# Kernel optimization log

Hardware: AMD Instinct MI355X
Metric: run time of the kernel (lower is better)

## Reference

```python
import jax, jax.numpy as jnp
import numpy as np

H = 64          # hidden_size
IN = 6          # input_size
PREDICT = 10    # predict_size


def _lstm_cell(x_t, h, c, Wih, Whh, bih, bhh):
    # PyTorch gate order: i, f, g, o ; gates = x W_ih^T + b_ih + h W_hh^T + b_hh
    g = x_t @ Wih.T + bih + h @ Whh.T + bhh            # [B, 4H]
    i, f, gg, o = jnp.split(g, 4, axis=-1)
    c_new = jax.nn.sigmoid(f) * c + jax.nn.sigmoid(i) * jnp.tanh(gg)
    h_new = jax.nn.sigmoid(o) * jnp.tanh(c_new)
    return h_new, c_new


def setup_inputs() -> dict:
    key = jax.random.key(0)
    ks = jax.random.split(key, 12)
    B, T = 4096, 1024
    s = 1.0 / np.sqrt(H)  # torch default uniform init bound
    u = lambda k, shape: jax.random.uniform(k, shape, jnp.float32, -s, s)
    return {
        "x": jax.random.normal(ks[0], (B, T, IN), jnp.float32),
        "W_ih0": u(ks[1], (4 * H, IN)),
        "W_hh0": u(ks[2], (4 * H, H)),
        "b_ih0": u(ks[3], (4 * H,)),
        "b_hh0": u(ks[4], (4 * H,)),
        "W_ih1": u(ks[5], (4 * H, H)),
        "W_hh1": u(ks[6], (4 * H, H)),
        "b_ih1": u(ks[7], (4 * H,)),
        "b_hh1": u(ks[8], (4 * H,)),
        "fc_w": u(ks[9], (IN, H)),
        "fc_b": u(ks[10], (IN,)),
    }


def reference(x, W_ih0, W_hh0, b_ih0, b_hh0, W_ih1, W_hh1, b_ih1, b_hh1, fc_w, fc_b):
    B = x.shape[0]
    zeros = jnp.zeros((B, H), x.dtype)
    init = (zeros, zeros, zeros, zeros)  # h0, c0, h1, c1

    def stacked_step(carry, x_t):
        h0, c0, h1, c1 = carry
        h0, c0 = _lstm_cell(x_t, h0, c0, W_ih0, W_hh0, b_ih0, b_hh0)
        h1, c1 = _lstm_cell(h0, h1, c1, W_ih1, W_hh1, b_ih1, b_hh1)
        return (h0, c0, h1, c1), None

    # Encoder: scan over time (batch_first -> transpose to [T, B, IN])
    carry, _ = jax.lax.scan(stacked_step, init, jnp.swapaxes(x, 0, 1))

    def dec_step(state, _):
        dec_in, c = state
        c, _ = stacked_step(c, dec_in)
        pred = c[0 + 2] @ fc_w.T + fc_b  # top-layer h -> [B, IN]
        return (pred, c), pred

    dec_in0 = x[:, -1, :]
    _, preds = jax.lax.scan(dec_step, (dec_in0, carry), None, length=PREDICT)
    return jnp.swapaxes(preds, 0, 1)  # [B, PREDICT, IN]
```

## Files before the change

kernel.cpp:

```cpp
#include <hip/hip_runtime.h>

#define T_SEQ   1024
#define INDIM   6
#define HDIM    64
#define NPRED   10
#define CHNK    128
#define S0      72
#define NROWS   16

typedef __bf16         bf16x8 __attribute__((ext_vector_type(8)));
typedef float          f32x4  __attribute__((ext_vector_type(4)));
typedef float          f32x2  __attribute__((ext_vector_type(2)));
typedef unsigned short us4    __attribute__((ext_vector_type(4)));

#define MFMA16(a, b, c) __builtin_amdgcn_mfma_f32_16x16x32_bf16((a), (b), (c), 0, 0, 0)

static __device__ __forceinline__ float bf2f(unsigned short b) {
  union { unsigned int u; float f; } v; v.u = ((unsigned int)b) << 16; return v.f;
}
static __device__ __forceinline__ unsigned short f2bf(float f) {
  union { __bf16 b; unsigned short u; } v; v.b = (__bf16)f; return v.u;
}

template <bool F32>
__global__ __launch_bounds__(512, 2)
void lstm2_pipe(const void* __restrict__ xv,
                const void* __restrict__ Wih0v,
                const void* __restrict__ Whh0v,
                const void* __restrict__ bih0v,
                const void* __restrict__ bhh0v,
                const void* __restrict__ Wih1v,
                const void* __restrict__ Whh1v,
                const void* __restrict__ bih1v,
                const void* __restrict__ bhh1v,
                const void* __restrict__ fcwv,
                const void* __restrict__ fcbv,
                void* __restrict__ outv)
{
  {
    const unsigned short* w0u = (const unsigned short*)Wih0v;
    int votes = 0;
#pragma unroll
    for (int i = 0; i < 16; ++i) {
      const unsigned e = (w0u[2 * i] >> 7) & 0xFF;
      votes += (e >= 0x80 || e <= 0x40) ? 1 : 0;
    }
    if ((votes >= 4) != F32) return;
  }

  __shared__ __align__(16) unsigned short A0[2][NROWS * S0];
  __shared__ __align__(16) unsigned short A1[2][NROWS * S0];
  __shared__ __align__(16) unsigned short XB2[NROWS * CHNK * 8];
  __shared__ __align__(16) unsigned short XD[NROWS * 8];
  __shared__ __align__(16) unsigned short ZPAD[8];
  __shared__ __align__(16) unsigned short FCW[INDIM * HDIM];
  __shared__ float FCB[INDIM];

  const int tid   = threadIdx.x;
  const int lane  = tid & 63;
  const int wave  = tid >> 6;
  const bool isA  = (wave < 4);
  const int  wv4  = wave & 3;
  const int  q    = lane >> 4;
  const int  n    = lane & 15;
  const int  u    = 16 * wv4 + n;
  const int rbase = blockIdx.x * NROWS;

  {
    unsigned short* p0 = &A0[0][0];
    unsigned short* p1 = &A1[0][0];
    for (int i = tid; i < 2 * NROWS * S0; i += 512) { p0[i] = 0; p1[i] = 0; }
    for (int i = tid; i < NROWS * 8; i += 512) XD[i] = 0;
    if (tid < 8) ZPAD[tid] = 0;
  }
  for (int i = tid; i < INDIM * HDIM; i += 512) {
    if constexpr (F32) FCW[i] = f2bf(((const float*)fcwv)[i]);
    else               FCW[i] = ((const unsigned short*)fcwv)[i];
  }
  if (tid < INDIM) {
    if constexpr (F32) FCB[tid] = ((const float*)fcbv)[tid];
    else               FCB[tid] = bf2f(((const unsigned short*)fcbv)[tid]);
  }

  auto ld1 = [&](const void* p, int i) -> float {
    if constexpr (F32) return ((const float*)p)[i];
    else               return bf2f(((const unsigned short*)p)[i]);
  };
  auto ld8 = [&](const void* W, int off) -> bf16x8 {
    union { unsigned short us[8]; bf16x8 v; } t;
    if constexpr (F32) {
      const float* p = (const float*)W + off;
#pragma unroll
      for (int j = 0; j < 8; ++j) t.us[j] = f2bf(p[j]);
    } else {
      t.v = *(const bf16x8*)((const unsigned short*)W + off);
    }
    return t.v;
  };

  auto load_chunk = [&](int t0c) {
    for (int c = tid; c < NROWS * CHNK; c += 512) {
      const int row = c >> 7;
      const int t   = c & (CHNK - 1);
      int4 o;
      if constexpr (F32) {
        const float* p = (const float*)xv + ((size_t)(rbase + row) * T_SEQ + (t0c + t)) * INDIM;
        const float2 v0 = *(const float2*)(p);
        const float2 v1 = *(const float2*)(p + 2);
        const float2 v2 = *(const float2*)(p + 4);
        union { unsigned short us[8]; int4 v; } tt;
        tt.us[0] = f2bf(v0.x); tt.us[1] = f2bf(v0.y);
        tt.us[2] = f2bf(v1.x); tt.us[3] = f2bf(v1.y);
        tt.us[4] = f2bf(v2.x); tt.us[5] = f2bf(v2.y);
        tt.us[6] = 0;          tt.us[7] = 0;
        o = tt.v;
      } else {
        const unsigned short* p = (const unsigned short*)xv
            + ((size_t)(rbase + row) * T_SEQ + (t0c + t)) * INDIM;
        o.x = *(const unsigned int*)(p);
        o.y = *(const unsigned int*)(p + 2);
        o.z = *(const unsigned int*)(p + 4);
        o.w = 0;
      }
      *(int4*)((char*)XB2 + (((size_t)row * CHNK) + (t ^ (row & 7))) * 16) = o;
    }
  };

  load_chunk(0);

  const int dxr = tid / INDIM;
  const int dxk = tid - dxr * INDIM;

  __syncthreads();

  const int aOff  = n * S0 + 8 * q;
  const int hOffW = n * S0 + 16 * wv4 + 4 * q;
  const int bOff  = 16 * wv4 + 4 * q;

  auto xsrc_at = [&](int tc) -> const char* {
    return (q == 0)
        ? ((const char*)XB2 + (((size_t)n * CHNK) + (tc ^ (n & 7))) * 16)
        : (const char*)ZPAD;
  };

  f32x2 cc2[2]; cc2[0] = (f32x2){0.f, 0.f}; cc2[1] = (f32x2){0.f, 0.f};

  auto ldbias = [&](const void* b1, const void* b2, int gt) -> f32x4 {
    f32x4 r;
#pragma unroll
    for (int j = 0; j < 4; ++j)
      r[j] = ld1(b1, 64 * gt + bOff + j) + ld1(b2, 64 * gt + bOff + j);
    return r;
  };

  const f32x2 C1   = {-1.442695040888963f, -1.442695040888963f};
  const f32x2 C2   = {-2.885390081777927f, -2.885390081777927f};
  const f32x2 onep = {1.0f, 1.0f};

  auto act4 = [&](const f32x4 gI, const f32x4 gF, const f32x4 gG, const f32x4 gO,
                  unsigned short* dst) {
    unsigned int w2[2];
#pragma unroll
    for (int p = 0; p < 2; ++p) {
      f32x2 vI, vF, vG, vO;
      vI.x = gI[2 * p]; vI.y = gI[2 * p + 1];
      vF.x = gF[2 * p]; vF.y = gF[2 * p + 1];
      vG.x = gG[2 * p]; vG.y = gG[2 * p + 1];
      vO.x = gO[2 * p]; vO.y = gO[2 * p + 1];
      const f32x2 aF = vF * C1;
      const f32x2 aI = vI * C1;
      const f32x2 aG = vG * C2;
      const f32x2 aO = vO * C1;
      f32x2 Ae, Be, Ge, Oe;
      Ae.x = __builtin_amdgcn_exp2f(aF.x); Ae.y = __builtin_amdgcn_exp2f(aF.y);
      Be.x = __builtin_amdgcn_exp2f(aI.x); Be.y = __builtin_amdgcn_exp2f(aI.y);
      Ge.x = __builtin_amdgcn_exp2f(aG.x); Ge.y = __builtin_amdgcn_exp2f(aG.y);
      Oe.x = __builtin_amdgcn_exp2f(aO.x); Oe.y = __builtin_amdgcn_exp2f(aO.y);
      const f32x2 M1 = (onep + Be) * (onep + Ge);
      const f32x2 t2 = onep + Ae;
      const f32x2 nm = cc2[p] * M1 + (onep - Ge) * t2;
      const f32x2 den = t2 * M1;
      f32x2 rd; rd.x = __builtin_amdgcn_rcpf(den.x); rd.y = __builtin_amdgcn_rcpf(den.y);
      const f32x2 cn = nm * rd;
      cc2[p] = cn;
      const f32x2 aE = cn * C2;
      f32x2 Ee; Ee.x = __builtin_amdgcn_exp2f(aE.x); Ee.y = __builtin_amdgcn_exp2f(aE.y);
      const f32x2 dh = (onep + Ee) * (onep + Oe);
      f32x2 rh; rh.x = __builtin_amdgcn_rcpf(dh.x); rh.y = __builtin_amdgcn_rcpf(dh.y);
      const f32x2 hv = (onep - Ee) * rh;
      w2[p] = (unsigned int)f2bf(hv.x) | ((unsigned int)f2bf(hv.y) << 16);
    }
    uint2 pk; pk.x = w2[0]; pk.y = w2[1];
    *(uint2*)(dst + hOffW) = pk;
  };

  unsigned short* H0 = &A0[0][0];
  unsigned short* H1 = &A1[1][0];

  if (isA) {
    bf16x8 WA[12]; f32x4 bvA[4];
#pragma unroll
    for (int gt = 0; gt < 4; ++gt) {
      const int col = 64 * gt + u;
      WA[gt * 3 + 0] = ld8(Whh0v, col * HDIM + 8 * q);
      WA[gt * 3 + 1] = ld8(Whh0v, col * HDIM + 32 + 8 * q);
      union { unsigned short us[8]; bf16x8 v; } t2;
#pragma unroll
      for (int j = 0; j < 8; ++j) t2.us[j] = 0;
      if (q == 0) {
#pragma unroll
        for (int j = 0; j < INDIM; ++j) t2.us[j] = f2bf(ld1(Wih0v, col * INDIM + j));
      }
      WA[gt * 3 + 2] = t2.v;
      bvA[gt] = ldbias(bih0v, bhh0v, gt);
    }

    int t0v = 0;
    for (int i = 0; i <= T_SEQ; ++i) {
      if (i > 0 && i < T_SEQ && (i & (CHNK - 1)) == 0) {
        load_chunk(i);
        __syncthreads();
        t0v = i;
      }
      const int cur = i & 1;
      if (i < T_SEQ) {
        const unsigned short* A0c = &A0[cur][0];
        unsigned short*       A0n = &A0[cur ^ 1][0];
        const bf16x8 f0 = *(const bf16x8*)(A0c + aOff);
        const bf16x8 f1 = *(const bf16x8*)(A0c + aOff + 32);
        const bf16x8 f2 = *(const bf16x8*)(xsrc_at(i - t0v));
        __builtin_amdgcn_s_setprio(1);
        f32x4 g0 = MFMA16(WA[0], f0, bvA[0]); g0 = MFMA16(WA[1],  f1, g0); g0 = MFMA16(WA[2],  f2, g0);
        f32x4 g1 = MFMA16(WA[3], f0, bvA[1]); g1 = MFMA16(WA[4],  f1, g1); g1 = MFMA16(WA[5],  f2, g1);
        f32x4 g2 = MFMA16(WA[6], f0, bvA[2]); g2 = MFMA16(WA[7],  f1, g2); g2 = MFMA16(WA[8],  f2, g2);
        f32x4 g3 = MFMA16(WA[9], f0, bvA[3]); g3 = MFMA16(WA[10], f1, g3); g3 = MFMA16(WA[11], f2, g3);
        __builtin_amdgcn_s_setprio(0);
        act4(g0, g1, g2, g3, A0n);
      }
      __syncthreads();
    }
    if (tid < 96)
      XD[dxr * 8 + dxk] = XB2[((size_t)dxr * CHNK + (127 ^ (dxr & 7))) * 8 + dxk];
    __syncthreads();
    for (int d = 0; d < NPRED; ++d) {
      const bf16x8 fa0 = *(const bf16x8*)(H0 + aOff);
      const bf16x8 fa1 = *(const bf16x8*)(H0 + aOff + 32);
      const bf16x8 fa2 = *(const bf16x8*)((q == 0) ? ((const char*)XD + n * 16)
                                                   : (const char*)ZPAD);
      __syncthreads();
      {
        f32x4 g0 = MFMA16(WA[0], fa0, bvA[0]); g0 = MFMA16(WA[1],  fa1, g0); g0 = MFMA16(WA[2],  fa2, g0);
        f32x4 g1 = MFMA16(WA[3], fa0, bvA[1]); g1 = MFMA16(WA[4],  fa1, g1); g1 = MFMA16(WA[5],  fa2, g1);
        f32x4 g2 = MFMA16(WA[6], fa0, bvA[2]); g2 = MFMA16(WA[7],  fa1, g2); g2 = MFMA16(WA[8],  fa2, g2);
        f32x4 g3 = MFMA16(WA[9], fa0, bvA[3]); g3 = MFMA16(WA[10], fa1, g3); g3 = MFMA16(WA[11], fa2, g3);
        act4(g0, g1, g2, g3, H0);
      }
      __syncthreads();
      __syncthreads();
      if (tid < 96) {
        const unsigned short* h1row = H1 + dxr * S0;
        const int4* hp = (const int4*)h1row;
        const int4* wp = (const int4*)(&FCW[dxk * HDIM]);
        float s = FCB[dxk];
#pragma unroll
        for (int i8 = 0; i8 < 8; ++i8) {
          const int4 hv = hp[i8];
          const int4 wv2 = wp[i8];
          const unsigned int hu[4] = {(unsigned)hv.x, (unsigned)hv.y, (unsigned)hv.z, (unsigned)hv.w};
          const unsigned int wu[4] = {(unsigned)wv2.x, (unsigned)wv2.y, (unsigned)wv2.z, (unsigned)wv2.w};
#pragma unroll
          for (int k2 = 0; k2 < 4; ++k2) {
            union { unsigned int uu; float ff; } hl, hh2, wl, wh;
            hl.uu = hu[k2] << 16; hh2.uu = hu[k2] & 0xFFFF0000u;
            wl.uu = wu[k2] << 16; wh.uu  = wu[k2] & 0xFFFF0000u;
            s += hl.ff * wl.ff + hh2.ff * wh.ff;
          }
        }
        const unsigned short pb = f2bf(s);
        const size_t idx = (size_t)(rbase + dxr) * (NPRED * INDIM) + (size_t)d * INDIM + dxk;
        if constexpr (F32) ((float*)outv)[idx] = s;
        else               ((unsigned short*)outv)[idx] = pb;
        XD[dxr * 8 + dxk] = pb;
      }
      __syncthreads();
    }
  } else {
    bf16x8 WB[16]; f32x4 bvB[4];
#pragma unroll
    for (int gt = 0; gt < 4; ++gt) {
      const int col = 64 * gt + u;
      WB[gt * 4 + 0] = ld8(Wih1v, col * HDIM + 8 * q);
      WB[gt * 4 + 1] = ld8(Wih1v, col * HDIM + 32 + 8 * q);
      WB[gt * 4 + 2] = ld8(Whh1v, col * HDIM + 8 * q);
      WB[gt * 4 + 3] = ld8(Whh1v, col * HDIM + 32 + 8 * q);
      bvB[gt] = ldbias(bih1v, bhh1v, gt);
    }

    for (int i = 0; i <= T_SEQ; ++i) {
      if (i > 0 && i < T_SEQ && (i & (CHNK - 1)) == 0) {
        load_chunk(i);
        __syncthreads();
      }
      const int cur = i & 1;
      if (i >= 1) {
        const unsigned short* A0c = &A0[cur][0];
        const unsigned short* A1c = &A1[cur][0];
        unsigned short*       A1n = &A1[cur ^ 1][0];
        const bf16x8 h0a = *(const bf16x8*)(A0c + aOff);
        const bf16x8 h0b = *(const bf16x8*)(A0c + aOff + 32);
        const bf16x8 r0  = *(const bf16x8*)(A1c + aOff);
        const bf16x8 r1  = *(const bf16x8*)(A1c + aOff + 32);
        __builtin_amdgcn_s_setprio(1);
        f32x4 g0 = MFMA16(WB[0],  h0a, bvB[0]); g0 = MFMA16(WB[1],  h0b, g0); g0 = MFMA16(WB[2],  r0, g0); g0 = MFMA16(WB[3],  r1, g0);
        f32x4 g1 = MFMA16(WB[4],  h0a, bvB[1]); g1 = MFMA16(WB[5],  h0b, g1); g1 = MFMA16(WB[6],  r0, g1); g1 = MFMA16(WB[7],  r1, g1);
        f32x4 g2 = MFMA16(WB[8],  h0a, bvB[2]); g2 = MFMA16(WB[9],  h0b, g2); g2 = MFMA16(WB[10], r0, g2); g2 = MFMA16(WB[11], r1, g2);
        f32x4 g3 = MFMA16(WB[12], h0a, bvB[3]); g3 = MFMA16(WB[13], h0b, g3); g3 = MFMA16(WB[14], r0, g3); g3 = MFMA16(WB[15], r1, g3);
        __builtin_amdgcn_s_setprio(0);
        act4(g0, g1, g2, g3, A1n);
      }
      __syncthreads();
    }
    __syncthreads();
    for (int d = 0; d < NPRED; ++d) {
      const bf16x8 fr0 = *(const bf16x8*)(H1 + aOff);
      const bf16x8 fr1 = *(const bf16x8*)(H1 + aOff + 32);
      __syncthreads();
      __syncthreads();
      {
        const bf16x8 h0a = *(const bf16x8*)(H0 + aOff);
        const bf16x8 h0b = *(const bf16x8*)(H0 + aOff + 32);
        f32x4 g0 = MFMA16(WB[0],  h0a, bvB[0]); g0 = MFMA16(WB[1],  h0b, g0); g0 = MFMA16(WB[2],  fr0, g0); g0 = MFMA16(WB[3],  fr1, g0);
        f32x4 g1 = MFMA16(WB[4],  h0a, bvB[1]); g1 = MFMA16(WB[5],  h0b, g1); g1 = MFMA16(WB[6],  fr0, g1); g1 = MFMA16(WB[7],  fr1, g1);
        f32x4 g2 = MFMA16(WB[8],  h0a, bvB[2]); g2 = MFMA16(WB[9],  h0b, g2); g2 = MFMA16(WB[10], fr0, g2); g2 = MFMA16(WB[11], fr1, g2);
        f32x4 g3 = MFMA16(WB[12], h0a, bvB[3]); g3 = MFMA16(WB[13], h0b, g3); g3 = MFMA16(WB[14], fr0, g3); g3 = MFMA16(WB[15], fr1, g3);
        act4(g0, g1, g2, g3, H1);
      }
      __syncthreads();
      __syncthreads();
    }
  }
}

extern "C" void kernel_launch(void* const* d_in, const int* in_sizes, int n_in,
                              void* d_out, int out_size, void* d_ws, size_t ws_size,
                              hipStream_t stream) {
  (void)in_sizes; (void)n_in; (void)d_ws; (void)ws_size; (void)out_size;
  const void* x    = d_in[0];
  const void* Wih0 = d_in[1];
  const void* Whh0 = d_in[2];
  const void* bih0 = d_in[3];
  const void* bhh0 = d_in[4];
  const void* Wih1 = d_in[5];
  const void* Whh1 = d_in[6];
  const void* bih1 = d_in[7];
  const void* bhh1 = d_in[8];
  const void* fcw  = d_in[9];
  const void* fcb  = d_in[10];
  lstm2_pipe<true><<<dim3(4096 / NROWS), dim3(512), 0, stream>>>(
      x, Wih0, Whh0, bih0, bhh0, Wih1, Whh1, bih1, bhh1, fcw, fcb, d_out);
  lstm2_pipe<false><<<dim3(4096 / NROWS), dim3(512), 0, stream>>>(
      x, Wih0, Whh0, bih0, bhh0, Wih1, Whh1, bih1, bhh1, fcw, fcb, d_out);
}
```

Before: 873.0 us.

## Collapse each LSTM layer into one wave with windowed ring-buffer synchronization

Each 16-row block now runs on two waves (128 threads) instead of eight. One wave computes all 256 gate columns of layer 0 and the other all columns of layer 1, with every weight fragment held in registers. Layer 0 writes its hidden states into a 16-deep shared ring, and the two layers meet at a block barrier only once per 8-step window, with layer 1 lagging one window behind. This removes the per-timestep __syncthreads that the eight-wave split needed. The cost is 4x more serial MFMA and activation work per wave, lower in-block parallelism, and heavier register pressure, with fewer threads available to hide latency.

```diff
diff --git a/kernel.cpp b/kernel.cpp
--- a/kernel.cpp
+++ b/kernel.cpp
@@ -4,16 +4,18 @@
 #define INDIM   6
 #define HDIM    64
 #define NPRED   10
-#define CHNK    128
+#define CHNK    64
 #define S0      72
 #define NROWS   16
+#define RD      16
+#define WIN     8
 
 typedef __bf16         bf16x8 __attribute__((ext_vector_type(8)));
 typedef float          f32x4  __attribute__((ext_vector_type(4)));
 typedef float          f32x2  __attribute__((ext_vector_type(2)));
-typedef unsigned short us4    __attribute__((ext_vector_type(4)));
 
 #define MFMA16(a, b, c) __builtin_amdgcn_mfma_f32_16x16x32_bf16((a), (b), (c), 0, 0, 0)
+#define MEMBAR() asm volatile("" ::: "memory")
 
 static __device__ __forceinline__ float bf2f(unsigned short b) {
   union { unsigned int u; float f; } v; v.u = ((unsigned int)b) << 16; return v.f;
@@ -23,7 +25,7 @@
 }
 
 template <bool F32>
-__global__ __launch_bounds__(512, 2)
+__global__ __launch_bounds__(128, 1)
 void lstm2_pipe(const void* __restrict__ xv,
                 const void* __restrict__ Wih0v,
                 const void* __restrict__ Whh0v,
@@ -48,9 +50,10 @@
     if ((votes >= 4) != F32) return;
   }
 
-  __shared__ __align__(16) unsigned short A0[2][NROWS * S0];
-  __shared__ __align__(16) unsigned short A1[2][NROWS * S0];
+  __shared__ __align__(16) unsigned short RING[RD * NROWS * S0];
+  __shared__ __align__(16) unsigned short H1B[2 * NROWS * S0];
   __shared__ __align__(16) unsigned short XB2[NROWS * CHNK * 8];
+  __shared__ __align__(16) float BIAS1[4 * HDIM];
   __shared__ __align__(16) unsigned short XD[NROWS * 8];
   __shared__ __align__(16) unsigned short ZPAD[8];
   __shared__ __align__(16) unsigned short FCW[INDIM * HDIM];
@@ -58,29 +61,10 @@
 
   const int tid   = threadIdx.x;
   const int lane  = tid & 63;
-  const int wave  = tid >> 6;
-  const bool isA  = (wave < 4);
-  const int  wv4  = wave & 3;
+  const bool isA  = (tid < 64);
   const int  q    = lane >> 4;
   const int  n    = lane & 15;
-  const int  u    = 16 * wv4 + n;
   const int rbase = blockIdx.x * NROWS;
-
-  {
-    unsigned short* p0 = &A0[0][0];
-    unsigned short* p1 = &A1[0][0];
-    for (int i = tid; i < 2 * NROWS * S0; i += 512) { p0[i] = 0; p1[i] = 0; }
-    for (int i = tid; i < NROWS * 8; i += 512) XD[i] = 0;
-    if (tid < 8) ZPAD[tid] = 0;
-  }
-  for (int i = tid; i < INDIM * HDIM; i += 512) {
-    if constexpr (F32) FCW[i] = f2bf(((const float*)fcwv)[i]);
-    else               FCW[i] = ((const unsigned short*)fcwv)[i];
-  }
-  if (tid < INDIM) {
-    if constexpr (F32) FCB[tid] = ((const float*)fcbv)[tid];
-    else               FCB[tid] = bf2f(((const unsigned short*)fcbv)[tid]);
-  }
 
   auto ld1 = [&](const void* p, int i) -> float {
     if constexpr (F32) return ((const float*)p)[i];
@@ -98,9 +82,69 @@
     return t.v;
   };
 
-  auto load_chunk = [&](int t0c) {
-    for (int c = tid; c < NROWS * CHNK; c += 512) {
-      const int row = c >> 7;
+  {
+    const int4 z = {0, 0, 0, 0};
+    for (int i = tid; i < (2 * NROWS * S0) / 8; i += 128) ((int4*)H1B)[i] = z;
+    if (tid < (NROWS * 8) / 8) ((int4*)XD)[tid] = z;
+    if (tid < 8) ZPAD[tid] = 0;
+  }
+  for (int i = tid; i < 4 * HDIM; i += 128) BIAS1[i] = ld1(bih1v, i) + ld1(bhh1v, i);
+  for (int i = tid; i < INDIM * HDIM; i += 128) {
+    if constexpr (F32) FCW[i] = f2bf(((const float*)fcwv)[i]);
+    else               FCW[i] = ((const unsigned short*)fcwv)[i];
+  }
+  if (tid < INDIM) {
+    if constexpr (F32) FCB[tid] = ((const float*)fcbv)[tid];
+    else               FCB[tid] = bf2f(((const unsigned short*)fcbv)[tid]);
+  }
+
+  const int aOff = n * S0 + 8 * q;
+  const int hW   = n * S0 + 4 * q;
+
+  const f32x2 C1   = {-1.442695040888963f, -1.442695040888963f};
+  const f32x2 C2   = {-2.885390081777927f, -2.885390081777927f};
+  const f32x2 onep = {1.0f, 1.0f};
+
+  auto act4 = [&](const f32x4 gI, const f32x4 gF, const f32x4 gG, const f32x4 gO,
+                  unsigned short* dst, f32x2* cc) {
+    unsigned int w2[2];
+#pragma unroll
+    for (int p = 0; p < 2; ++p) {
+      f32x2 vI, vF, vG, vO;
+      vI.x = gI[2 * p]; vI.y = gI[2 * p + 1];
+      vF.x = gF[2 * p]; vF.y = gF[2 * p + 1];
+      vG.x = gG[2 * p]; vG.y = gG[2 * p + 1];
+      vO.x = gO[2 * p]; vO.y = gO[2 * p + 1];
+      const f32x2 aF = vF * C1;
+      const f32x2 aI = vI * C1;
+      const f32x2 aG = vG * C2;
+      const f32x2 aO = vO * C1;
+      f32x2 Ae, Be, Ge, Oe;
+      Ae.x = __builtin_amdgcn_exp2f(aF.x); Ae.y = __builtin_amdgcn_exp2f(aF.y);
+      Be.x = __builtin_amdgcn_exp2f(aI.x); Be.y = __builtin_amdgcn_exp2f(aI.y);
+      Ge.x = __builtin_amdgcn_exp2f(aG.x); Ge.y = __builtin_amdgcn_exp2f(aG.y);
+      Oe.x = __builtin_amdgcn_exp2f(aO.x); Oe.y = __builtin_amdgcn_exp2f(aO.y);
+      const f32x2 M1 = (onep + Be) * (onep + Ge);
+      const f32x2 t2 = onep + Ae;
+      const f32x2 nm = cc[p] * M1 + (onep - Ge) * t2;
+      const f32x2 den = t2 * M1;
+      f32x2 rd; rd.x = __builtin_amdgcn_rcpf(den.x); rd.y = __builtin_amdgcn_rcpf(den.y);
+      const f32x2 cn = nm * rd;
+      cc[p] = cn;
+      const f32x2 aE = cn * C2;
+      f32x2 Ee; Ee.x = __builtin_amdgcn_exp2f(aE.x); Ee.y = __builtin_amdgcn_exp2f(aE.y);
+      const f32x2 dh = (onep + Ee) * (onep + Oe);
+      f32x2 rh; rh.x = __builtin_amdgcn_rcpf(dh.x); rh.y = __builtin_amdgcn_rcpf(dh.y);
+      const f32x2 hv = (onep - Ee) * rh;
+      w2[p] = (unsigned int)f2bf(hv.x) | ((unsigned int)f2bf(hv.y) << 16);
+    }
+    uint2 pk; pk.x = w2[0]; pk.y = w2[1];
+    *(uint2*)(dst + hW) = pk;
+  };
+
+  auto stage = [&](int t0c) {
+    for (int c = lane; c < NROWS * CHNK; c += 64) {
+      const int row = c >> 6;
       const int t   = c & (CHNK - 1);
       int4 o;
       if constexpr (F32) {
@@ -124,144 +168,183 @@
       }
       *(int4*)((char*)XB2 + (((size_t)row * CHNK) + (t ^ (row & 7))) * 16) = o;
     }
+    MEMBAR();
   };
 
-  load_chunk(0);
-
-  const int dxr = tid / INDIM;
-  const int dxk = tid - dxr * INDIM;
-
-  __syncthreads();
-
-  const int aOff  = n * S0 + 8 * q;
-  const int hOffW = n * S0 + 16 * wv4 + 4 * q;
-  const int bOff  = 16 * wv4 + 4 * q;
-
-  auto xsrc_at = [&](int tc) -> const char* {
-    return (q == 0)
-        ? ((const char*)XB2 + (((size_t)n * CHNK) + (tc ^ (n & 7))) * 16)
-        : (const char*)ZPAD;
-  };
-
-  f32x2 cc2[2]; cc2[0] = (f32x2){0.f, 0.f}; cc2[1] = (f32x2){0.f, 0.f};
-
-  auto ldbias = [&](const void* b1, const void* b2, int gt) -> f32x4 {
-    f32x4 r;
-#pragma unroll
-    for (int j = 0; j < 4; ++j)
-      r[j] = ld1(b1, 64 * gt + bOff + j) + ld1(b2, 64 * gt + bOff + j);
-    return r;
-  };
-
-  const f32x2 C1   = {-1.442695040888963f, -1.442695040888963f};
-  const f32x2 C2   = {-2.885390081777927f, -2.885390081777927f};
-  const f32x2 onep = {1.0f, 1.0f};
-
-  auto act4 = [&](const f32x4 gI, const f32x4 gF, const f32x4 gG, const f32x4 gO,
-                  unsigned short* dst) {
-    unsigned int w2[2];
-#pragma unroll
-    for (int p = 0; p < 2; ++p) {
-      f32x2 vI, vF, vG, vO;
-      vI.x = gI[2 * p]; vI.y = gI[2 * p + 1];
-      vF.x = gF[2 * p]; vF.y = gF[2 * p + 1];
-      vG.x = gG[2 * p]; vG.y = gG[2 * p + 1];
-      vO.x = gO[2 * p]; vO.y = gO[2 * p + 1];
-      const f32x2 aF = vF * C1;
-      const f32x2 aI = vI * C1;
-      const f32x2 aG = vG * C2;
-      const f32x2 aO = vO * C1;
-      f32x2 Ae, Be, Ge, Oe;
-      Ae.x = __builtin_amdgcn_exp2f(aF.x); Ae.y = __builtin_amdgcn_exp2f(aF.y);
-      Be.x = __builtin_amdgcn_exp2f(aI.x); Be.y = __builtin_amdgcn_exp2f(aI.y);
-      Ge.x = __builtin_amdgcn_exp2f(aG.x); Ge.y = __builtin_amdgcn_exp2f(aG.y);
-      Oe.x = __builtin_amdgcn_exp2f(aO.x); Oe.y = __builtin_amdgcn_exp2f(aO.y);
-      const f32x2 M1 = (onep + Be) * (onep + Ge);
-      const f32x2 t2 = onep + Ae;
-      const f32x2 nm = cc2[p] * M1 + (onep - Ge) * t2;
-      const f32x2 den = t2 * M1;
-      f32x2 rd; rd.x = __builtin_amdgcn_rcpf(den.x); rd.y = __builtin_amdgcn_rcpf(den.y);
-      const f32x2 cn = nm * rd;
-      cc2[p] = cn;
-      const f32x2 aE = cn * C2;
-      f32x2 Ee; Ee.x = __builtin_amdgcn_exp2f(aE.x); Ee.y = __builtin_amdgcn_exp2f(aE.y);
-      const f32x2 dh = (onep + Ee) * (onep + Oe);
-      f32x2 rh; rh.x = __builtin_amdgcn_rcpf(dh.x); rh.y = __builtin_amdgcn_rcpf(dh.y);
-      const f32x2 hv = (onep - Ee) * rh;
-      w2[p] = (unsigned int)f2bf(hv.x) | ((unsigned int)f2bf(hv.y) << 16);
-    }
-    uint2 pk; pk.x = w2[0]; pk.y = w2[1];
-    *(uint2*)(dst + hOffW) = pk;
-  };
-
-  unsigned short* H0 = &A0[0][0];
-  unsigned short* H1 = &A1[1][0];
-
   if (isA) {
-    bf16x8 WA[12]; f32x4 bvA[4];
-#pragma unroll
-    for (int gt = 0; gt < 4; ++gt) {
-      const int col = 64 * gt + u;
-      WA[gt * 3 + 0] = ld8(Whh0v, col * HDIM + 8 * q);
-      WA[gt * 3 + 1] = ld8(Whh0v, col * HDIM + 32 + 8 * q);
-      union { unsigned short us[8]; bf16x8 v; } t2;
-#pragma unroll
-      for (int j = 0; j < 8; ++j) t2.us[j] = 0;
-      if (q == 0) {
-#pragma unroll
-        for (int j = 0; j < INDIM; ++j) t2.us[j] = f2bf(ld1(Wih0v, col * INDIM + j));
-      }
-      WA[gt * 3 + 2] = t2.v;
-      bvA[gt] = ldbias(bih0v, bhh0v, gt);
-    }
-
-    int t0v = 0;
-    for (int i = 0; i <= T_SEQ; ++i) {
-      if (i > 0 && i < T_SEQ && (i & (CHNK - 1)) == 0) {
-        load_chunk(i);
-        __syncthreads();
-        t0v = i;
-      }
-      const int cur = i & 1;
-      if (i < T_SEQ) {
-        const unsigned short* A0c = &A0[cur][0];
-        unsigned short*       A0n = &A0[cur ^ 1][0];
-        const bf16x8 f0 = *(const bf16x8*)(A0c + aOff);
-        const bf16x8 f1 = *(const bf16x8*)(A0c + aOff + 32);
-        const bf16x8 f2 = *(const bf16x8*)(xsrc_at(i - t0v));
-        __builtin_amdgcn_s_setprio(1);
-        f32x4 g0 = MFMA16(WA[0], f0, bvA[0]); g0 = MFMA16(WA[1],  f1, g0); g0 = MFMA16(WA[2],  f2, g0);
-        f32x4 g1 = MFMA16(WA[3], f0, bvA[1]); g1 = MFMA16(WA[4],  f1, g1); g1 = MFMA16(WA[5],  f2, g1);
-        f32x4 g2 = MFMA16(WA[6], f0, bvA[2]); g2 = MFMA16(WA[7],  f1, g2); g2 = MFMA16(WA[8],  f2, g2);
-        f32x4 g3 = MFMA16(WA[9], f0, bvA[3]); g3 = MFMA16(WA[10], f1, g3); g3 = MFMA16(WA[11], f2, g3);
-        __builtin_amdgcn_s_setprio(0);
-        act4(g0, g1, g2, g3, A0n);
-      }
-      __syncthreads();
-    }
-    if (tid < 96)
-      XD[dxr * 8 + dxk] = XB2[((size_t)dxr * CHNK + (127 ^ (dxr & 7))) * 8 + dxk];
-    __syncthreads();
+    bf16x8 W0A[16], W1A[16], WXA[16]; f32x4 bvA[16];
+#pragma unroll
+    for (int g = 0; g < 4; ++g) {
+#pragma unroll
+      for (int j = 0; j < 4; ++j) {
+        const int gj = g * 4 + j;
+        const int rowW = 64 * g + 16 * j + n;
+        W0A[gj] = ld8(Whh0v, rowW * HDIM + 8 * q);
+        W1A[gj] = ld8(Whh0v, rowW * HDIM + 32 + 8 * q);
+        union { unsigned short us[8]; bf16x8 v; } t2;
+#pragma unroll
+        for (int jj = 0; jj < 8; ++jj) t2.us[jj] = 0;
+        if (q == 0) {
+#pragma unroll
+          for (int jj = 0; jj < INDIM; ++jj) t2.us[jj] = f2bf(ld1(Wih0v, rowW * INDIM + jj));
+        }
+        WXA[gj] = t2.v;
+        const int bb = 64 * g + 16 * j + 4 * q;
+        f32x4 bv;
+#pragma unroll
+        for (int jj = 0; jj < 4; ++jj) bv[jj] = ld1(bih0v, bb + jj) + ld1(bhh0v, bb + jj);
+        bvA[gj] = bv;
+      }
+    }
+
+    f32x2 ccA[8];
+#pragma unroll
+    for (int i = 0; i < 8; ++i) ccA[i] = (f32x2){0.f, 0.f};
+    bf16x8 f0, f1;
+    {
+      union { unsigned short us[8]; bf16x8 v; } z;
+#pragma unroll
+      for (int jj = 0; jj < 8; ++jj) z.us[jj] = 0;
+      f0 = z.v; f1 = z.v;
+    }
+
+#pragma unroll 1
+    for (int w = 0; w <= T_SEQ / WIN; ++w) {
+      __syncthreads();
+      if (w < T_SEQ / WIN) {
+        const int tb = w * WIN;
+        if ((tb & (CHNK - 1)) == 0) stage(tb);
+#pragma unroll 1
+        for (int s = 0; s < WIN; ++s) {
+          const int t = tb + s;
+          MEMBAR();
+          bf16x8 xf;
+          if (q == 0) xf = *(const bf16x8*)((const char*)XB2
+                           + (((size_t)n * CHNK) + ((t & (CHNK - 1)) ^ (n & 7))) * 16);
+          else        xf = *(const bf16x8*)ZPAD;
+          unsigned short* dst = &RING[(t & (RD - 1)) * (NROWS * S0)];
+          bf16x8 f0n, f1n;
+#pragma unroll
+          for (int j = 0; j < 4; ++j) {
+            f32x4 g0 = MFMA16(W0A[0*4+j], f0, bvA[0*4+j]); g0 = MFMA16(W1A[0*4+j], f1, g0); g0 = MFMA16(WXA[0*4+j], xf, g0);
+            f32x4 g1 = MFMA16(W0A[1*4+j], f0, bvA[1*4+j]); g1 = MFMA16(W1A[1*4+j], f1, g1); g1 = MFMA16(WXA[1*4+j], xf, g1);
+            f32x4 g2 = MFMA16(W0A[2*4+j], f0, bvA[2*4+j]); g2 = MFMA16(W1A[2*4+j], f1, g2); g2 = MFMA16(WXA[2*4+j], xf, g2);
+            f32x4 g3 = MFMA16(W0A[3*4+j], f0, bvA[3*4+j]); g3 = MFMA16(W1A[3*4+j], f1, g3); g3 = MFMA16(WXA[3*4+j], xf, g3);
+            act4(g0, g1, g2, g3, dst + 16 * j, &ccA[2 * j]);
+            if (j == 1) { MEMBAR(); f0n = *(const bf16x8*)(dst + aOff); }
+          }
+          MEMBAR();
+          f1n = *(const bf16x8*)(dst + aOff + 32);
+          f0 = f0n; f1 = f1n;
+        }
+      }
+    }
+    if (lane < 16)
+      *(int4*)(XD + lane * 8) = *(const int4*)((const char*)XB2
+          + (((size_t)lane * CHNK) + ((CHNK - 1) ^ (lane & 7))) * 16);
+    unsigned short* H0d = &RING[(RD - 1) * (NROWS * S0)];
+#pragma unroll 1
     for (int d = 0; d < NPRED; ++d) {
-      const bf16x8 fa0 = *(const bf16x8*)(H0 + aOff);
-      const bf16x8 fa1 = *(const bf16x8*)(H0 + aOff + 32);
-      const bf16x8 fa2 = *(const bf16x8*)((q == 0) ? ((const char*)XD + n * 16)
-                                                   : (const char*)ZPAD);
-      __syncthreads();
-      {
-        f32x4 g0 = MFMA16(WA[0], fa0, bvA[0]); g0 = MFMA16(WA[1],  fa1, g0); g0 = MFMA16(WA[2],  fa2, g0);
-        f32x4 g1 = MFMA16(WA[3], fa0, bvA[1]); g1 = MFMA16(WA[4],  fa1, g1); g1 = MFMA16(WA[5],  fa2, g1);
-        f32x4 g2 = MFMA16(WA[6], fa0, bvA[2]); g2 = MFMA16(WA[7],  fa1, g2); g2 = MFMA16(WA[8],  fa2, g2);
-        f32x4 g3 = MFMA16(WA[9], fa0, bvA[3]); g3 = MFMA16(WA[10], fa1, g3); g3 = MFMA16(WA[11], fa2, g3);
-        act4(g0, g1, g2, g3, H0);
-      }
-      __syncthreads();
-      __syncthreads();
-      if (tid < 96) {
-        const unsigned short* h1row = H1 + dxr * S0;
+      __syncthreads();
+      MEMBAR();
+      const bf16x8 fa0 = *(const bf16x8*)(H0d + aOff);
+      const bf16x8 fa1 = *(const bf16x8*)(H0d + aOff + 32);
+      bf16x8 fx;
+      if (q == 0) fx = *(const bf16x8*)((const char*)XD + n * 16);
+      else        fx = *(const bf16x8*)ZPAD;
+#pragma unroll
+      for (int j = 0; j < 4; ++j) {
+        f32x4 g0 = MFMA16(W0A[0*4+j], fa0, bvA[0*4+j]); g0 = MFMA16(W1A[0*4+j], fa1, g0); g0 = MFMA16(WXA[0*4+j], fx, g0);
+        f32x4 g1 = MFMA16(W0A[1*4+j], fa0, bvA[1*4+j]); g1 = MFMA16(W1A[1*4+j], fa1, g1); g1 = MFMA16(WXA[1*4+j], fx, g1);
+        f32x4 g2 = MFMA16(W0A[2*4+j], fa0, bvA[2*4+j]); g2 = MFMA16(W1A[2*4+j], fa1, g2); g2 = MFMA16(WXA[2*4+j], fx, g2);
+        f32x4 g3 = MFMA16(W0A[3*4+j], fa0, bvA[3*4+j]); g3 = MFMA16(W1A[3*4+j], fa1, g3); g3 = MFMA16(WXA[3*4+j], fx, g3);
+        act4(g0, g1, g2, g3, H0d + 16 * j, &ccA[2 * j]);
+      }
+      __syncthreads();
+    }
+  } else {
+    bf16x8 Wi0[16], Wi1[16], Wh0[16], Wh1[16];
+#pragma unroll
+    for (int g = 0; g < 4; ++g) {
+#pragma unroll
+      for (int j = 0; j < 4; ++j) {
+        const int gj = g * 4 + j;
+        const int rowW = 64 * g + 16 * j + n;
+        Wi0[gj] = ld8(Wih1v, rowW * HDIM + 8 * q);
+        Wi1[gj] = ld8(Wih1v, rowW * HDIM + 32 + 8 * q);
+        Wh0[gj] = ld8(Whh1v, rowW * HDIM + 8 * q);
+        Wh1[gj] = ld8(Whh1v, rowW * HDIM + 32 + 8 * q);
+      }
+    }
+    f32x2 ccB[8];
+#pragma unroll
+    for (int i = 0; i < 8; ++i) ccB[i] = (f32x2){0.f, 0.f};
+
+#pragma unroll 1
+    for (int w = 0; w <= T_SEQ / WIN; ++w) {
+      __syncthreads();
+      if (w >= 1) {
+        const int tb = (w - 1) * WIN;
+#pragma unroll 1
+        for (int s = 0; s < WIN; ++s) {
+          const int t = tb + s;
+          MEMBAR();
+          const unsigned short* h0s = &RING[(t & (RD - 1)) * (NROWS * S0)];
+          const unsigned short* h1s = &H1B[((t + 1) & 1) * (NROWS * S0)];
+          unsigned short*       dst = &H1B[(t & 1) * (NROWS * S0)];
+          const bf16x8 a0 = *(const bf16x8*)(h0s + aOff);
+          const bf16x8 a1 = *(const bf16x8*)(h0s + aOff + 32);
+          const bf16x8 b0 = *(const bf16x8*)(h1s + aOff);
+          const bf16x8 b1 = *(const bf16x8*)(h1s + aOff + 32);
+#pragma unroll
+          for (int j = 0; j < 4; ++j) {
+            const f32x4 c0 = *(const f32x4*)(&BIAS1[0 * 64 + 16 * j + 4 * q]);
+            const f32x4 c1 = *(const f32x4*)(&BIAS1[1 * 64 + 16 * j + 4 * q]);
+            const f32x4 c2 = *(const f32x4*)(&BIAS1[2 * 64 + 16 * j + 4 * q]);
+            const f32x4 c3 = *(const f32x4*)(&BIAS1[3 * 64 + 16 * j + 4 * q]);
+            f32x4 g0 = MFMA16(Wi0[0*4+j], a0, c0); g0 = MFMA16(Wi1[0*4+j], a1, g0); g0 = MFMA16(Wh0[0*4+j], b0, g0); g0 = MFMA16(Wh1[0*4+j], b1, g0);
+            f32x4 g1 = MFMA16(Wi0[1*4+j], a0, c1); g1 = MFMA16(Wi1[1*4+j], a1, g1); g1 = MFMA16(Wh0[1*4+j], b0, g1); g1 = MFMA16(Wh1[1*4+j], b1, g1);
+            f32x4 g2 = MFMA16(Wi0[2*4+j], a0, c2); g2 = MFMA16(Wi1[2*4+j], a1, g2); g2 = MFMA16(Wh0[2*4+j], b0, g2); g2 = MFMA16(Wh1[2*4+j], b1, g2);
+            f32x4 g3 = MFMA16(Wi0[3*4+j], a0, c3); g3 = MFMA16(Wi1[3*4+j], a1, g3); g3 = MFMA16(Wh0[3*4+j], b0, g3); g3 = MFMA16(Wh1[3*4+j], b1, g3);
+            act4(g0, g1, g2, g3, dst + 16 * j, &ccB[2 * j]);
+          }
+        }
+      }
+    }
+    int p = 1;
+#pragma unroll 1
+    for (int d = 0; d < NPRED; ++d) {
+      __syncthreads();
+      __syncthreads();
+      MEMBAR();
+      const unsigned short* h0s = &RING[(RD - 1) * (NROWS * S0)];
+      const unsigned short* h1s = &H1B[p * (NROWS * S0)];
+      unsigned short*       dst = &H1B[(p ^ 1) * (NROWS * S0)];
+      const bf16x8 a0 = *(const bf16x8*)(h0s + aOff);
+      const bf16x8 a1 = *(const bf16x8*)(h0s + aOff + 32);
+      const bf16x8 b0 = *(const bf16x8*)(h1s + aOff);
+      const bf16x8 b1 = *(const bf16x8*)(h1s + aOff + 32);
+#pragma unroll
+      for (int j = 0; j < 4; ++j) {
+        const f32x4 c0 = *(const f32x4*)(&BIAS1[0 * 64 + 16 * j + 4 * q]);
+        const f32x4 c1 = *(const f32x4*)(&BIAS1[1 * 64 + 16 * j + 4 * q]);
+        const f32x4 c2 = *(const f32x4*)(&BIAS1[2 * 64 + 16 * j + 4 * q]);
+        const f32x4 c3 = *(const f32x4*)(&BIAS1[3 * 64 + 16 * j + 4 * q]);
+        f32x4 g0 = MFMA16(Wi0[0*4+j], a0, c0); g0 = MFMA16(Wi1[0*4+j], a1, g0); g0 = MFMA16(Wh0[0*4+j], b0, g0); g0 = MFMA16(Wh1[0*4+j], b1, g0);
+        f32x4 g1 = MFMA16(Wi0[1*4+j], a0, c1); g1 = MFMA16(Wi1[1*4+j], a1, g1); g1 = MFMA16(Wh0[1*4+j], b0, g1); g1 = MFMA16(Wh1[1*4+j], b1, g1);
+        f32x4 g2 = MFMA16(Wi0[2*4+j], a0, c2); g2 = MFMA16(Wi1[2*4+j], a1, g2); g2 = MFMA16(Wh0[2*4+j], b0, g2); g2 = MFMA16(Wh1[2*4+j], b1, g2);
+        f32x4 g3 = MFMA16(Wi0[3*4+j], a0, c3); g3 = MFMA16(Wi1[3*4+j], a1, g3); g3 = MFMA16(Wh0[3*4+j], b0, g3); g3 = MFMA16(Wh1[3*4+j], b1, g3);
+        act4(g0, g1, g2, g3, dst + 16 * j, &ccB[2 * j]);
+      }
+      MEMBAR();
+#pragma unroll 1
+      for (int e = lane; e < 96; e += 64) {
+        const int row = e / INDIM;
+        const int k   = e - row * INDIM;
+        const unsigned short* h1row = dst + row * S0;
         const int4* hp = (const int4*)h1row;
-        const int4* wp = (const int4*)(&FCW[dxk * HDIM]);
-        float s = FCB[dxk];
+        const int4* wp = (const int4*)(&FCW[k * HDIM]);
+        float sacc = FCB[k];
 #pragma unroll
         for (int i8 = 0; i8 < 8; ++i8) {
           const int4 hv = hp[i8];
@@ -273,70 +356,16 @@
             union { unsigned int uu; float ff; } hl, hh2, wl, wh;
             hl.uu = hu[k2] << 16; hh2.uu = hu[k2] & 0xFFFF0000u;
             wl.uu = wu[k2] << 16; wh.uu  = wu[k2] & 0xFFFF0000u;
-            s += hl.ff * wl.ff + hh2.ff * wh.ff;
+            sacc += hl.ff * wl.ff + hh2.ff * wh.ff;
           }
         }
-        const unsigned short pb = f2bf(s);
-        const size_t idx = (size_t)(rbase + dxr) * (NPRED * INDIM) + (size_t)d * INDIM + dxk;
-        if constexpr (F32) ((float*)outv)[idx] = s;
+        const unsigned short pb = f2bf(sacc);
+        const size_t idx = (size_t)(rbase + row) * (NPRED * INDIM) + (size_t)d * INDIM + k;
+        if constexpr (F32) ((float*)outv)[idx] = sacc;
         else               ((unsigned short*)outv)[idx] = pb;
-        XD[dxr * 8 + dxk] = pb;
-      }
-      __syncthreads();
-    }
-  } else {
-    bf16x8 WB[16]; f32x4 bvB[4];
-#pragma unroll
-    for (int gt = 0; gt < 4; ++gt) {
-      const int col = 64 * gt + u;
-      WB[gt * 4 + 0] = ld8(Wih1v, col * HDIM + 8 * q);
-      WB[gt * 4 + 1] = ld8(Wih1v, col * HDIM + 32 + 8 * q);
-      WB[gt * 4 + 2] = ld8(Whh1v, col * HDIM + 8 * q);
-      WB[gt * 4 + 3] = ld8(Whh1v, col * HDIM + 32 + 8 * q);
-      bvB[gt] = ldbias(bih1v, bhh1v, gt);
-    }
-
-    for (int i = 0; i <= T_SEQ; ++i) {
-      if (i > 0 && i < T_SEQ && (i & (CHNK - 1)) == 0) {
-        load_chunk(i);
-        __syncthreads();
-      }
-      const int cur = i & 1;
-      if (i >= 1) {
-        const unsigned short* A0c = &A0[cur][0];
-        const unsigned short* A1c = &A1[cur][0];
-        unsigned short*       A1n = &A1[cur ^ 1][0];
-        const bf16x8 h0a = *(const bf16x8*)(A0c + aOff);
-        const bf16x8 h0b = *(const bf16x8*)(A0c + aOff + 32);
-        const bf16x8 r0  = *(const bf16x8*)(A1c + aOff);
-        const bf16x8 r1  = *(const bf16x8*)(A1c + aOff + 32);
-        __builtin_amdgcn_s_setprio(1);
-        f32x4 g0 = MFMA16(WB[0],  h0a, bvB[0]); g0 = MFMA16(WB[1],  h0b, g0); g0 = MFMA16(WB[2],  r0, g0); g0 = MFMA16(WB[3],  r1, g0);
-        f32x4 g1 = MFMA16(WB[4],  h0a, bvB[1]); g1 = MFMA16(WB[5],  h0b, g1); g1 = MFMA16(WB[6],  r0, g1); g1 = MFMA16(WB[7],  r1, g1);
-        f32x4 g2 = MFMA16(WB[8],  h0a, bvB[2]); g2 = MFMA16(WB[9],  h0b, g2); g2 = MFMA16(WB[10], r0, g2); g2 = MFMA16(WB[11], r1, g2);
-        f32x4 g3 = MFMA16(WB[12], h0a, bvB[3]); g3 = MFMA16(WB[13], h0b, g3); g3 = MFMA16(WB[14], r0, g3); g3 = MFMA16(WB[15], r1, g3);
-        __builtin_amdgcn_s_setprio(0);
-        act4(g0, g1, g2, g3, A1n);
-      }
-      __syncthreads();
-    }
-    __syncthreads();
-    for (int d = 0; d < NPRED; ++d) {
-      const bf16x8 fr0 = *(const bf16x8*)(H1 + aOff);
-      const bf16x8 fr1 = *(const bf16x8*)(H1 + aOff + 32);
-      __syncthreads();
-      __syncthreads();
-      {
-        const bf16x8 h0a = *(const bf16x8*)(H0 + aOff);
-        const bf16x8 h0b = *(const bf16x8*)(H0 + aOff + 32);
-        f32x4 g0 = MFMA16(WB[0],  h0a, bvB[0]); g0 = MFMA16(WB[1],  h0b, g0); g0 = MFMA16(WB[2],  fr0, g0); g0 = MFMA16(WB[3],  fr1, g0);
-        f32x4 g1 = MFMA16(WB[4],  h0a, bvB[1]); g1 = MFMA16(WB[5],  h0b, g1); g1 = MFMA16(WB[6],  fr0, g1); g1 = MFMA16(WB[7],  fr1, g1);
-        f32x4 g2 = MFMA16(WB[8],  h0a, bvB[2]); g2 = MFMA16(WB[9],  h0b, g2); g2 = MFMA16(WB[10], fr0, g2); g2 = MFMA16(WB[11], fr1, g2);
-        f32x4 g3 = MFMA16(WB[12], h0a, bvB[3]); g3 = MFMA16(WB[13], h0b, g3); g3 = MFMA16(WB[14], fr0, g3); g3 = MFMA16(WB[15], fr1, g3);
-        act4(g0, g1, g2, g3, H1);
-      }
-      __syncthreads();
-      __syncthreads();
+        XD[row * 8 + k] = pb;
+      }
+      p ^= 1;
     }
   }
 }
@@ -356,8 +385,8 @@
   const void* bhh1 = d_in[8];
   const void* fcw  = d_in[9];
   const void* fcb  = d_in[10];
-  lstm2_pipe<true><<<dim3(4096 / NROWS), dim3(512), 0, stream>>>(
+  lstm2_pipe<true><<<dim3(4096 / NROWS), dim3(128), 0, stream>>>(
       x, Wih0, Whh0, bih0, bhh0, Wih1, Whh1, bih1, bhh1, fcw, fcb, d_out);
-  lstm2_pipe<false><<<dim3(4096 / NROWS), dim3(512), 0, stream>>>(
+  lstm2_pipe<false><<<dim3(4096 / NROWS), dim3(128), 0, stream>>>(
       x, Wih0, Whh0, bih0, bhh0, Wih1, Whh1, bih1, bhh1, fcw, fcb, d_out);
 }
```

Result: slower. 1.739 ms (+99.2%).
